# Optimization experiments

Hardware: AMD Instinct MI355X
Metric: run time of the kernel (lower is better)

The kernel has to match this reference:

```python
import jax, jax.numpy as jnp
import numpy as np

N_NODES = 50000
N_EDGES = 800000
N_GRAPHS = 256
F_IN = 75  # num_features_xd


def _lin_params(key, fan_in, fan_out):
    kw, kb = jax.random.split(key)
    s = 1.0 / np.sqrt(fan_in)
    W = jax.random.uniform(kw, (fan_in, fan_out), jnp.float32, -s, s)
    b = jax.random.uniform(kb, (fan_out,), jnp.float32, -s, s)
    return W, b


def setup_inputs() -> dict:
    key = jax.random.key(0)
    ks = jax.random.split(key, 8)
    x = jax.random.normal(ks[0], (N_NODES, F_IN), jnp.float32)
    edge_index = jax.random.randint(ks[1], (2, N_EDGES), 0, N_NODES, jnp.int32)
    batch = jnp.sort(jax.random.randint(ks[2], (N_NODES,), 0, N_GRAPHS, jnp.int32))
    W1, b1 = _lin_params(ks[3], F_IN, F_IN)            # conv1: 75 -> 75
    W2, b2 = _lin_params(ks[4], F_IN, 2 * F_IN)        # conv2: 75 -> 150
    W3, b3 = _lin_params(ks[5], 2 * F_IN, 4 * F_IN)    # conv3: 150 -> 300
    Wg1, bg1 = _lin_params(ks[6], 4 * F_IN, 1024)      # fc_g1: 300 -> 1024
    Wg2, bg2 = _lin_params(ks[7], 1024, 128)           # fc_g2: 1024 -> 128
    return dict(x=x, edge_index=edge_index, batch=batch,
                W1=W1, b1=b1, W2=W2, b2=b2, W3=W3, b3=b3,
                Wg1=Wg1, bg1=bg1, Wg2=Wg2, bg2=bg2)


def gcn_conv(x, W, b, src, dst, n):
    """PyG GCNConv: out = D^{-1/2}(A+I)D^{-1/2} X W + b (symmetric norm, self loops)."""
    h = x @ W                                   # [n, out]
    loop = jnp.arange(n, dtype=src.dtype)
    s = jnp.concatenate([src, loop])            # [E+n]
    d = jnp.concatenate([dst, loop])
    deg = jax.ops.segment_sum(jnp.ones(s.shape[0], x.dtype), d, num_segments=n)
    dinv = jnp.where(deg > 0, jax.lax.rsqrt(jnp.maximum(deg, 1e-12)), 0.0)
    norm = dinv[s] * dinv[d]                    # [E+n]
    out = jax.ops.segment_sum(norm[:, None] * h[s], d, num_segments=n)
    return out + b


def reference(x, edge_index, batch, W1, b1, W2, b2, W3, b3, Wg1, bg1, Wg2, bg2):
    src, dst = edge_index[0], edge_index[1]
    n = x.shape[0]
    h = jax.nn.relu(gcn_conv(x, W1, b1, src, dst, n))
    h = jax.nn.relu(gcn_conv(h, W2, b2, src, dst, n))
    h = jax.nn.relu(gcn_conv(h, W3, b3, src, dst, n))
    g = jax.ops.segment_max(h, batch, num_segments=N_GRAPHS)  # global max pool
    g = jax.nn.relu(g @ Wg1 + bg1)
    # dropout is identity in eval mode
    return g @ Wg2 + bg2
```

## Files before the change

### kernel.cpp

```cpp
#include <hip/hip_runtime.h>
#include <math.h>

#define SCAN_B 1024
#define LDST 40

typedef __attribute__((ext_vector_type(8))) short short8v;
typedef __attribute__((ext_vector_type(8))) unsigned short ushort8v;
typedef __attribute__((ext_vector_type(4))) float f32x4;

static inline int ceil_div_i(long long a, int b) { return (int)((a + b - 1) / b); }

__device__ __forceinline__ unsigned short f2bf(float x) {
    unsigned int u = __float_as_uint(x);
    u += 0x7fffu + ((u >> 16) & 1u);
    return (unsigned short)(u >> 16);
}
__device__ __forceinline__ float bf2f(unsigned short h) {
    return __uint_as_float(((unsigned int)h) << 16);
}


__global__ __launch_bounds__(256) void k_count(const int* __restrict__ dst, int E,
                                               int* __restrict__ cnt) {
    int i = blockIdx.x * blockDim.x + threadIdx.x;
    if (i < E) atomicAdd(&cnt[dst[i]], 1);
}

__global__ __launch_bounds__(256) void k_dinv(const int* __restrict__ cnt,
                                              float* __restrict__ dinv, int N) {
    int i = blockIdx.x * blockDim.x + threadIdx.x;
    if (i < N) dinv[i] = (float)(1.0 / sqrt((double)(cnt[i] + 1)));
}

__global__ __launch_bounds__(256) void k_scan1(const int* __restrict__ cnt,
                                               int* __restrict__ rowptr,
                                               int* __restrict__ bsum, int N) {
    __shared__ int s[256];
    int tid = threadIdx.x;
    int base = blockIdx.x * SCAN_B + tid * 4;
    int a0 = (base + 0 < N) ? cnt[base + 0] : 0;
    int a1 = (base + 1 < N) ? cnt[base + 1] : 0;
    int a2 = (base + 2 < N) ? cnt[base + 2] : 0;
    int a3 = (base + 3 < N) ? cnt[base + 3] : 0;
    int tsum = a0 + a1 + a2 + a3;
    s[tid] = tsum;
    __syncthreads();
    for (int off = 1; off < 256; off <<= 1) {
        int val = 0;
        if (tid >= off) val = s[tid - off];
        __syncthreads();
        if (tid >= off) s[tid] += val;
        __syncthreads();
    }
    int texcl = s[tid] - tsum;
    if (tid == 255) bsum[blockIdx.x] = s[255];
    if (base + 0 < N) rowptr[base + 0] = texcl;
    if (base + 1 < N) rowptr[base + 1] = texcl + a0;
    if (base + 2 < N) rowptr[base + 2] = texcl + a0 + a1;
    if (base + 3 < N) rowptr[base + 3] = texcl + a0 + a1 + a2;
}

__global__ __launch_bounds__(256) void k_scan2(int* __restrict__ bsum, int NB) {
    __shared__ int s[256];
    int tid = threadIdx.x;
    int v = (tid < NB) ? bsum[tid] : 0;
    s[tid] = v;
    __syncthreads();
    for (int off = 1; off < 256; off <<= 1) {
        int val = 0;
        if (tid >= off) val = s[tid - off];
        __syncthreads();
        if (tid >= off) s[tid] += val;
        __syncthreads();
    }
    if (tid < NB) bsum[tid] = s[tid] - v;
}

__global__ __launch_bounds__(256) void k_scan3(int* __restrict__ rowptr,
                                               const int* __restrict__ bsum, int N, int E) {
    int i = blockIdx.x * blockDim.x + threadIdx.x;
    if (i < N) rowptr[i] += bsum[i >> 10];
    if (i == 0) rowptr[N] = E;
}

__global__ __launch_bounds__(256) void k_fill(const int* __restrict__ src,
                                              const int* __restrict__ dst, int E,
                                              const int* __restrict__ rowptr,
                                              int* __restrict__ fill,
                                              const float* __restrict__ dinv,
                                              int* __restrict__ col,
                                              float* __restrict__ ew) {
    int e = blockIdx.x * blockDim.x + threadIdx.x;
    if (e >= E) return;
    int s = src[e], d = dst[e];
    int pos = atomicAdd(&fill[d], 1);
    int idx = rowptr[d] + pos;
    col[idx] = s;
    ew[idx] = dinv[s] * dinv[d];
}


__global__ __launch_bounds__(256) void k_xpad(const float* __restrict__ x,
                                              float* __restrict__ xp, int N, int F, int XS) {
    int i = blockIdx.x * blockDim.x + threadIdx.x;
    int v = i / XS, c = i - v * XS;
    if (v >= N) return;
    xp[i] = (c < F) ? x[(size_t)v * F + c] : 0.f;
}


template <int BF16IN, int CHUNKS, int SLOTS, int UNR>
__global__ __launch_bounds__(256) void k_gather_s(const void* __restrict__ Xv,
                                                  const int* __restrict__ rowptr,
                                                  const int* __restrict__ col,
                                                  const float* __restrict__ ew,
                                                  const float* __restrict__ dinv,
                                                  float* __restrict__ T, int N,
                                                  int XS, int KPf) {
    const int v = blockIdx.x * 4 + (threadIdx.x >> 6);
    const int lane = threadIdx.x & 63;
    if (v >= N) return;
    constexpr int VW = BF16IN ? 8 : 4;
    const int slot = lane / CHUNKS;
    const int chunk = lane - slot * CHUNKS;
    const bool act = lane < CHUNKS * SLOTS;
    const int f0 = chunk * VW;
    const float* Xf = (const float*)Xv;
    const unsigned short* Xb = (const unsigned short*)Xv;
    const float dv = dinv[v];
    const float s = dv * dv;

    float acc[VW];
#pragma unroll
    for (int u = 0; u < VW; u++) acc[u] = 0.f;
    if (slot == 0) {
        if (BF16IN) {
            ushort8v h = *(const ushort8v*)(Xb + (size_t)v * XS + f0);
#pragma unroll
            for (int u = 0; u < VW; u++) acc[u] = s * bf2f(h[u]);
        } else {
            f32x4 t4 = *(const f32x4*)(Xf + (size_t)v * XS + f0);
#pragma unroll
            for (int u = 0; u < VW; u++) acc[u] = s * t4[u];
        }
    }

    const int beg = rowptr[v], end = rowptr[v + 1];
    for (int jb = beg; jb < end; jb += 64) {
        const int nj = min(64, end - jb);
        int ec = 0;
        float emeta = 0.f;
        if (lane < nj) {
            ec = col[jb + lane];
            emeta = ew[jb + lane];
        }
        for (int e = 0; e < nj; e += SLOTS * UNR) {
            int cs[UNR];
            float ws[UNR];
            bool vs[UNR];
#pragma unroll
            for (int u = 0; u < UNR; u++) {
                int srcl = e + u * SLOTS + slot;
                vs[u] = act && (srcl < nj);
                int sl = srcl & 63;
                cs[u] = __shfl(ec, sl);
                ws[u] = __shfl(emeta, sl);
                if (!vs[u]) ws[u] = 0.f;
            }
            if (BF16IN) {
                ushort8v xv[UNR];
#pragma unroll
                for (int u = 0; u < UNR; u++) {
#pragma unroll
                    for (int k2 = 0; k2 < 8; k2++) xv[u][k2] = 0;
                    if (vs[u]) xv[u] = *(const ushort8v*)(Xb + (size_t)cs[u] * XS + f0);
                }
#pragma unroll
                for (int u = 0; u < UNR; u++)
#pragma unroll
                    for (int k2 = 0; k2 < VW; k2++)
                        acc[k2] = fmaf(ws[u], bf2f(xv[u][k2]), acc[k2]);
            } else {
                f32x4 xv[UNR];
#pragma unroll
                for (int u = 0; u < UNR; u++) {
                    xv[u] = (f32x4){0.f, 0.f, 0.f, 0.f};
                    if (vs[u]) xv[u] = *(const f32x4*)(Xf + (size_t)cs[u] * XS + f0);
                }
#pragma unroll
                for (int u = 0; u < UNR; u++)
#pragma unroll
                    for (int k2 = 0; k2 < VW; k2++)
                        acc[k2] = fmaf(ws[u], xv[u][k2], acc[k2]);
            }
        }
    }

#pragma unroll
    for (int k2 = 0; k2 < VW; k2++) {
        float t2 = acc[k2];
#pragma unroll
        for (int s2 = 1; s2 < SLOTS; s2++) t2 += __shfl(acc[k2], chunk + s2 * CHUNKS);
        acc[k2] = t2;
    }

    if (slot == 0 && f0 < KPf) {
        float* tv = T + (size_t)v * KPf + f0;
        f32x4 o0 = {acc[0], acc[1], acc[2], acc[3]};
        *(f32x4*)tv = o0;
        if (VW == 8) {
            f32x4 o1 = {acc[4], acc[5], acc[6], acc[7]};
            *(f32x4*)(tv + 4) = o1;
        }
    }
}


__global__ __launch_bounds__(256) void k_wsplit(const float* __restrict__ W,
                                                unsigned short* __restrict__ Wth,
                                                unsigned short* __restrict__ Wtl,
                                                int K, int Fout, int KP) {
    int i = blockIdx.x * blockDim.x + threadIdx.x;
    if (i >= Fout * KP) return;
    int c = i / KP, k = i - c * KP;
    float w = (k < K) ? W[(size_t)k * Fout + c] : 0.f;
    unsigned short h = f2bf(w);
    Wth[i] = h;
    Wtl[i] = f2bf(w - bf2f(h));
}


template <int MODE>
__global__ __launch_bounds__(256) void k_gemm_mfma(
    const float* __restrict__ A, int KPf,
    const unsigned short* __restrict__ Bth, const unsigned short* __restrict__ Btl,
    const float* __restrict__ bias, unsigned short* __restrict__ Cb, int CSbf,
    const int* __restrict__ batch, float* __restrict__ G,
    int N, int KP, int Fout) {
    __shared__ unsigned short sAh[128 * LDST];
    __shared__ unsigned short sAl[128 * LDST];
    __shared__ unsigned short sBh[128 * LDST];
    __shared__ unsigned short sBl[128 * LDST];
    __shared__ int sBatch[128];

    const int t = threadIdx.x;
    const int r0 = blockIdx.x * 128;
    const int c0 = blockIdx.y * 128;
    const int lane = t & 63;
    const int wv = t >> 6;
    const int wrow = (wv >> 1) * 64;
    const int wcol = (wv & 1) * 64;
    const int l15 = lane & 15;
    const int lk = (lane >> 4) * 8;
    const int nt = KP >> 5;

    const int srow = t >> 1;
    const int sseg = (t & 1) << 4;

    if (MODE == 1 && t < 128) sBatch[t] = (r0 + t < N) ? batch[r0 + t] : -1;

    const bool arow_ok = (r0 + srow) < N;
    const bool bcol_ok = (c0 + srow) < Fout;
    const float* aRow = A + (size_t)(r0 + srow) * KPf;
    const unsigned short* bhRow = Bth + (size_t)(c0 + srow) * KP;
    const unsigned short* blRow = Btl + (size_t)(c0 + srow) * KP;

    float av[16];
    ushort8v rbh0, rbh1, rbl0, rbl1;

    auto gload = [&](int kk) {
#pragma unroll
        for (int u = 0; u < 4; u++) {
            int gk = kk + sseg + u * 4;
            f32x4 f = {0.f, 0.f, 0.f, 0.f};
            if (arow_ok && gk < KPf) f = *(const f32x4*)&aRow[gk];
#pragma unroll
            for (int e = 0; e < 4; e++) av[u * 4 + e] = f[e];
        }
        if (bcol_ok) {
            const ushort8v* p = (const ushort8v*)&bhRow[kk + sseg];
            rbh0 = p[0];
            rbh1 = p[1];
            p = (const ushort8v*)&blRow[kk + sseg];
            rbl0 = p[0];
            rbl1 = p[1];
        } else {
#pragma unroll
            for (int e = 0; e < 8; e++) { rbh0[e] = 0; rbh1[e] = 0; rbl0[e] = 0; rbl1[e] = 0; }
        }
    };

    auto wlds = [&]() {
        int off = srow * LDST + sseg;
        ushort8v h0, h1, l0, l1;
#pragma unroll
        for (int e = 0; e < 8; e++) {
            unsigned short hh = f2bf(av[e]);
            h0[e] = hh;
            l0[e] = f2bf(av[e] - bf2f(hh));
        }
#pragma unroll
        for (int e = 0; e < 8; e++) {
            unsigned short hh = f2bf(av[8 + e]);
            h1[e] = hh;
            l1[e] = f2bf(av[8 + e] - bf2f(hh));
        }
        *(ushort8v*)&sAh[off] = h0;
        *(ushort8v*)&sAh[off + 8] = h1;
        *(ushort8v*)&sAl[off] = l0;
        *(ushort8v*)&sAl[off + 8] = l1;
        *(ushort8v*)&sBh[off] = rbh0;
        *(ushort8v*)&sBh[off + 8] = rbh1;
        *(ushort8v*)&sBl[off] = rbl0;
        *(ushort8v*)&sBl[off + 8] = rbl1;
    };

    f32x4 acc[4][4];
#pragma unroll
    for (int i = 0; i < 4; i++)
#pragma unroll
        for (int j = 0; j < 4; j++) acc[i][j] = (f32x4){0.f, 0.f, 0.f, 0.f};

    gload(0);
    for (int tc = 0; tc < nt; ++tc) {
        wlds();
        __syncthreads();
        if (tc + 1 < nt) gload((tc + 1) * 32);
        short8v ah[4], al[4];
#pragma unroll
        for (int i = 0; i < 4; i++) {
            int ro = (wrow + i * 16 + l15) * LDST + lk;
            ah[i] = *(const short8v*)&sAh[ro];
            al[i] = *(const short8v*)&sAl[ro];
        }
#pragma unroll
        for (int j = 0; j < 4; j++) {
            int co = (wcol + j * 16 + l15) * LDST + lk;
            short8v bh = *(const short8v*)&sBh[co];
            short8v bl = *(const short8v*)&sBl[co];
#pragma unroll
            for (int i = 0; i < 4; i++) {
                acc[i][j] = __builtin_amdgcn_mfma_f32_16x16x32_bf16(al[i], bh, acc[i][j], 0, 0, 0);
                acc[i][j] = __builtin_amdgcn_mfma_f32_16x16x32_bf16(ah[i], bl, acc[i][j], 0, 0, 0);
                acc[i][j] = __builtin_amdgcn_mfma_f32_16x16x32_bf16(ah[i], bh, acc[i][j], 0, 0, 0);
            }
        }
        __syncthreads();
    }

    if (MODE == 0) {
#pragma unroll
        for (int j = 0; j < 4; j++) {
            int gc = c0 + wcol + j * 16 + l15;
            if (gc >= CSbf) continue;
            float bv = (gc < Fout) ? bias[gc] : 0.f;
#pragma unroll
            for (int i = 0; i < 4; i++) {
                int rb = r0 + wrow + i * 16 + (lane >> 4) * 4;
#pragma unroll
                for (int q = 0; q < 4; q++) {
                    int gr = rb + q;
                    if (gr >= N) continue;
                    float vv = (gc < Fout) ? fmaxf(acc[i][j][q] + bv, 0.f) : 0.f;
                    Cb[(size_t)gr * CSbf + gc] = f2bf(vv);
                }
            }
        }
    } else {
#pragma unroll
        for (int j = 0; j < 4; j++) {
            int gc = c0 + wcol + j * 16 + l15;
            if (gc >= Fout) continue;
            float bv = bias[gc];
            int gcur = -1;
            float vmax = 0.f;
#pragma unroll
            for (int i = 0; i < 4; i++) {
                int lr = wrow + i * 16 + (lane >> 4) * 4;
#pragma unroll
                for (int q = 0; q < 4; q++) {
                    int g = sBatch[lr + q];
                    float vv = fmaxf(acc[i][j][q] + bv, 0.f);
                    if (g < 0) continue;
                    if (g != gcur) {
                        if (gcur >= 0)
                            atomicMax((int*)&G[(size_t)gcur * Fout + gc], __float_as_int(vmax));
                        gcur = g;
                        vmax = vv;
                    } else {
                        vmax = fmaxf(vmax, vv);
                    }
                }
            }
            if (gcur >= 0) atomicMax((int*)&G[(size_t)gcur * Fout + gc], __float_as_int(vmax));
        }
    }
}


__global__ __launch_bounds__(256) void k_fc1(const float* __restrict__ A,
                                             const float* __restrict__ W,
                                             const float* __restrict__ bias,
                                             float* __restrict__ C,
                                             int M, int K, int Nout) {
    __shared__ float sA[2 * 304];
    const int t = threadIdx.x;
    const int m0 = blockIdx.x * 2;
    const int oc = blockIdx.y * 256 + t;

    for (int i = t; i < 2 * K; i += 256) {
        int r = i / K, k = i - r * K;
        sA[r * 304 + k] = (m0 + r < M) ? A[(size_t)(m0 + r) * K + k] : 0.f;
    }
    __syncthreads();

    float acc0 = 0.f, acc1 = 0.f;
    int k = 0;
    for (; k + 8 <= K; k += 8) {
        float w[8];
#pragma unroll
        for (int u = 0; u < 8; u++) w[u] = W[(size_t)(k + u) * Nout + oc];
#pragma unroll
        for (int u = 0; u < 8; u++) {
            acc0 = fmaf(sA[k + u], w[u], acc0);
            acc1 = fmaf(sA[304 + k + u], w[u], acc1);
        }
    }
    for (; k < K; k++) {
        float w = W[(size_t)k * Nout + oc];
        acc0 = fmaf(sA[k], w, acc0);
        acc1 = fmaf(sA[304 + k], w, acc1);
    }
    float bv = bias[oc];
    if (m0 < M) C[(size_t)m0 * Nout + oc] = fmaxf(acc0 + bv, 0.f);
    if (m0 + 1 < M) C[(size_t)(m0 + 1) * Nout + oc] = fmaxf(acc1 + bv, 0.f);
}


__global__ __launch_bounds__(256) void k_fc2p(const float* __restrict__ A,
                                              const float* __restrict__ W,
                                              float* __restrict__ P,
                                              int M, int K, int Nout) {
    __shared__ float sA[2 * 256];
    const int t = threadIdx.x;
    const int m0 = blockIdx.x * 2;
    const int sk = blockIdx.y;
    const int k0 = sk * 256;
    const int row = t >> 7;
    const int oc = t & 127;

    for (int i = t; i < 2 * 256; i += 256) {
        int r = i >> 8, k = i & 255;
        sA[i] = (m0 + r < M) ? A[(size_t)(m0 + r) * K + k0 + k] : 0.f;
    }
    __syncthreads();

    const float* a = sA + row * 256;
    float acc = 0.f;
    for (int k = 0; k < 256; k += 8) {
        float w[8];
#pragma unroll
        for (int u = 0; u < 8; u++) w[u] = W[(size_t)(k0 + k + u) * Nout + oc];
#pragma unroll
        for (int u = 0; u < 8; u++) acc = fmaf(a[k + u], w[u], acc);
    }
    int m = m0 + row;
    if (m < M) P[((size_t)sk * M + m) * Nout + oc] = acc;
}

__global__ __launch_bounds__(256) void k_fc2r(const float* __restrict__ P,
                                              const float* __restrict__ bias,
                                              float* __restrict__ C,
                                              int M, int Nout, int SK) {
    int i = blockIdx.x * blockDim.x + threadIdx.x;
    if (i >= M * Nout) return;
    int oc = i % Nout;
    float acc = bias[oc];
    for (int s2 = 0; s2 < SK; s2++) acc += P[(size_t)s2 * M * Nout + i];
    C[i] = acc;
}


extern "C" void kernel_launch(void* const* d_in, const int* in_sizes, int n_in,
                              void* d_out, int out_size, void* d_ws, size_t ws_size,
                              hipStream_t stream) {
    const float* x     = (const float*)d_in[0];
    const int*   ei    = (const int*)d_in[1];
    const int*   batch = (const int*)d_in[2];
    const float* W1 = (const float*)d_in[3];
    const float* b1 = (const float*)d_in[4];
    const float* W2 = (const float*)d_in[5];
    const float* b2 = (const float*)d_in[6];
    const float* W3 = (const float*)d_in[7];
    const float* b3 = (const float*)d_in[8];
    const float* Wg1 = (const float*)d_in[9];
    const float* bg1 = (const float*)d_in[10];
    const float* Wg2 = (const float*)d_in[11];
    const float* bg2 = (const float*)d_in[12];

    const int N  = in_sizes[2];
    const int E  = in_sizes[1] / 2;
    const int F1 = in_sizes[4];
    const int F2 = in_sizes[6];
    const int F3 = in_sizes[8];
    const int H1 = in_sizes[10];
    const int OC = in_sizes[12];
    const int NG = out_size / OC;
    const int FIN = in_sizes[3] / F1;

    const int KP1 = 96,  KPf1 = 80;
    const int KP3 = 160, KPf3 = 152;
    const int XSP = 76;
    const int HS1 = 80;
    const int HS2 = 152;

    const int* src = ei;
    const int* dst = ei + E;

    char* base = (char*)d_ws;
    size_t off = 0;
    auto alloc = [&](size_t bytes) -> void* {
        void* p = base + off;
        off = (off + bytes + 255) & ~(size_t)255;
        return p;
    };
    int*   cnt    = (int*)alloc((size_t)N * 4);
    int*   fill   = (int*)alloc((size_t)N * 4);
    int*   rowptr = (int*)alloc((size_t)(N + 1) * 4);
    float* dinv   = (float*)alloc((size_t)N * 4);
    int*   bsum   = (int*)alloc(256 * 4);
    int*   col    = (int*)alloc((size_t)E * 4);
    float* ew     = (float*)alloc((size_t)E * 4);
    unsigned short* W1th = (unsigned short*)alloc((size_t)F1 * KP1 * 2);
    unsigned short* W1tl = (unsigned short*)alloc((size_t)F1 * KP1 * 2);
    unsigned short* W2th = (unsigned short*)alloc((size_t)F2 * KP1 * 2);
    unsigned short* W2tl = (unsigned short*)alloc((size_t)F2 * KP1 * 2);
    unsigned short* W3th = (unsigned short*)alloc((size_t)F3 * KP3 * 2);
    unsigned short* W3tl = (unsigned short*)alloc((size_t)F3 * KP3 * 2);
    float* Gb  = (float*)alloc((size_t)NG * F3 * 4);
    float* g1  = (float*)alloc((size_t)NG * H1 * 4);
    float* P2  = (float*)alloc((size_t)4 * NG * OC * 4);
    float* Tg  = (float*)alloc((size_t)N * KPf3 * 4);
    float* xp  = (float*)alloc((size_t)N * XSP * 4);
    unsigned short* H1b = (unsigned short*)alloc((size_t)N * HS1 * 2);
    unsigned short* H2b = (unsigned short*)alloc((size_t)N * HS2 * 2);

    hipMemsetAsync(cnt, 0, (size_t)N * 4, stream);
    hipMemsetAsync(fill, 0, (size_t)N * 4, stream);
    hipMemsetAsync(Gb, 0, (size_t)NG * F3 * 4, stream);

    k_count<<<ceil_div_i(E, 256), 256, 0, stream>>>(dst, E, cnt);
    k_dinv<<<ceil_div_i(N, 256), 256, 0, stream>>>(cnt, dinv, N);
    int NB = ceil_div_i(N, SCAN_B);
    k_scan1<<<NB, 256, 0, stream>>>(cnt, rowptr, bsum, N);
    k_scan2<<<1, 256, 0, stream>>>(bsum, NB);
    k_scan3<<<ceil_div_i(N, 256), 256, 0, stream>>>(rowptr, bsum, N, E);
    k_fill<<<ceil_div_i(E, 256), 256, 0, stream>>>(src, dst, E, rowptr, fill, dinv, col, ew);

    k_wsplit<<<ceil_div_i((long long)F1 * KP1, 256), 256, 0, stream>>>(W1, W1th, W1tl, FIN, F1, KP1);
    k_wsplit<<<ceil_div_i((long long)F2 * KP1, 256), 256, 0, stream>>>(W2, W2th, W2tl, F1, F2, KP1);
    k_wsplit<<<ceil_div_i((long long)F3 * KP3, 256), 256, 0, stream>>>(W3, W3th, W3tl, F2, F3, KP3);
    k_xpad<<<ceil_div_i((long long)N * XSP, 256), 256, 0, stream>>>(x, xp, N, FIN, XSP);

    dim3 blk(256);
    int gw = ceil_div_i(N, 4);
    int gx = ceil_div_i(N, 128);

    k_gather_s<0, 19, 3, 4><<<gw, blk, 0, stream>>>(xp, rowptr, col, ew, dinv, Tg,
                                                    N, XSP, KPf1);
    {
        dim3 g(gx, ceil_div_i(F1, 128));
        k_gemm_mfma<0><<<g, blk, 0, stream>>>(Tg, KPf1, W1th, W1tl, b1, H1b, HS1,
                                              nullptr, nullptr, N, KP1, F1);
    }
    k_gather_s<1, 10, 6, 2><<<gw, blk, 0, stream>>>(H1b, rowptr, col, ew, dinv, Tg,
                                                    N, HS1, KPf1);
    {
        dim3 g(gx, ceil_div_i(F2, 128));
        k_gemm_mfma<0><<<g, blk, 0, stream>>>(Tg, KPf1, W2th, W2tl, b2, H2b, HS2,
                                              nullptr, nullptr, N, KP1, F2);
    }
    k_gather_s<1, 19, 3, 4><<<gw, blk, 0, stream>>>(H2b, rowptr, col, ew, dinv, Tg,
                                                    N, HS2, KPf3);
    {
        dim3 g(gx, ceil_div_i(F3, 128));
        k_gemm_mfma<1><<<g, blk, 0, stream>>>(Tg, KPf3, W3th, W3tl, b3, nullptr, 0,
                                              batch, Gb, N, KP3, F3);
    }

    {
        dim3 g(ceil_div_i(NG, 2), H1 / 256);
        k_fc1<<<g, 256, 0, stream>>>(Gb, Wg1, bg1, g1, NG, F3, H1);
    }
    {
        dim3 g(ceil_div_i(NG, 2), 4);
        k_fc2p<<<g, 256, 0, stream>>>(g1, Wg2, P2, NG, H1, OC);
        k_fc2r<<<ceil_div_i((long long)NG * OC, 256), 256, 0, stream>>>(
            P2, bg2, (float*)d_out, NG, OC, 4);
    }
}
```

Baseline: 356.6 us.

## Fold symmetric GCN normalization into node features, drop per-edge weights

Factors the D^-1/2 A D^-1/2 normalization into per-node scaling: inputs are pre-scaled by dinv, the gather just sums neighbor rows, and the GEMM epilogue multiplies by dinv before bias and again after ReLU for the next layer. This removes the per-edge weight array, its writes in k_fill, its reads and shuffles in every gather, and turns FMAs into adds. The first-layer input is also converted to bf16 (stride 80), which halves gather traffic for layer 1 but adds rounding error on the raw input.

```diff
diff --git a/kernel.cpp b/kernel.cpp
--- a/kernel.cpp
+++ b/kernel.cpp
@@ -87,112 +87,77 @@
                                               const int* __restrict__ dst, int E,
                                               const int* __restrict__ rowptr,
                                               int* __restrict__ fill,
-                                              const float* __restrict__ dinv,
-                                              int* __restrict__ col,
-                                              float* __restrict__ ew) {
+                                              int* __restrict__ col) {
     int e = blockIdx.x * blockDim.x + threadIdx.x;
     if (e >= E) return;
     int s = src[e], d = dst[e];
     int pos = atomicAdd(&fill[d], 1);
-    int idx = rowptr[d] + pos;
-    col[idx] = s;
-    ew[idx] = dinv[s] * dinv[d];
-}
-
-
-__global__ __launch_bounds__(256) void k_xpad(const float* __restrict__ x,
-                                              float* __restrict__ xp, int N, int F, int XS) {
+    col[rowptr[d] + pos] = s;
+}
+
+
+__global__ __launch_bounds__(256) void k_xscale(const float* __restrict__ x,
+                                                const float* __restrict__ dinv,
+                                                unsigned short* __restrict__ xb,
+                                                int N, int F, int XS) {
     int i = blockIdx.x * blockDim.x + threadIdx.x;
     int v = i / XS, c = i - v * XS;
     if (v >= N) return;
-    xp[i] = (c < F) ? x[(size_t)v * F + c] : 0.f;
-}
-
-
-template <int BF16IN, int CHUNKS, int SLOTS, int UNR>
-__global__ __launch_bounds__(256) void k_gather_s(const void* __restrict__ Xv,
+    float val = (c < F) ? dinv[v] * x[(size_t)v * F + c] : 0.f;
+    xb[i] = f2bf(val);
+}
+
+
+template <int CHUNKS, int SLOTS, int UNR>
+__global__ __launch_bounds__(256) void k_gather_s(const unsigned short* __restrict__ Xb,
                                                   const int* __restrict__ rowptr,
                                                   const int* __restrict__ col,
-                                                  const float* __restrict__ ew,
-                                                  const float* __restrict__ dinv,
                                                   float* __restrict__ T, int N,
                                                   int XS, int KPf) {
     const int v = blockIdx.x * 4 + (threadIdx.x >> 6);
     const int lane = threadIdx.x & 63;
     if (v >= N) return;
-    constexpr int VW = BF16IN ? 8 : 4;
+    constexpr int VW = 8;
     const int slot = lane / CHUNKS;
     const int chunk = lane - slot * CHUNKS;
     const bool act = lane < CHUNKS * SLOTS;
     const int f0 = chunk * VW;
-    const float* Xf = (const float*)Xv;
-    const unsigned short* Xb = (const unsigned short*)Xv;
-    const float dv = dinv[v];
-    const float s = dv * dv;
 
     float acc[VW];
 #pragma unroll
     for (int u = 0; u < VW; u++) acc[u] = 0.f;
     if (slot == 0) {
-        if (BF16IN) {
-            ushort8v h = *(const ushort8v*)(Xb + (size_t)v * XS + f0);
-#pragma unroll
-            for (int u = 0; u < VW; u++) acc[u] = s * bf2f(h[u]);
-        } else {
-            f32x4 t4 = *(const f32x4*)(Xf + (size_t)v * XS + f0);
-#pragma unroll
-            for (int u = 0; u < VW; u++) acc[u] = s * t4[u];
-        }
+        ushort8v h = *(const ushort8v*)(Xb + (size_t)v * XS + f0);
+#pragma unroll
+        for (int u = 0; u < VW; u++) acc[u] = bf2f(h[u]);
     }
 
     const int beg = rowptr[v], end = rowptr[v + 1];
     for (int jb = beg; jb < end; jb += 64) {
         const int nj = min(64, end - jb);
         int ec = 0;
-        float emeta = 0.f;
-        if (lane < nj) {
-            ec = col[jb + lane];
-            emeta = ew[jb + lane];
-        }
+        if (lane < nj) ec = col[jb + lane];
         for (int e = 0; e < nj; e += SLOTS * UNR) {
             int cs[UNR];
-            float ws[UNR];
             bool vs[UNR];
 #pragma unroll
             for (int u = 0; u < UNR; u++) {
                 int srcl = e + u * SLOTS + slot;
                 vs[u] = act && (srcl < nj);
-                int sl = srcl & 63;
-                cs[u] = __shfl(ec, sl);
-                ws[u] = __shfl(emeta, sl);
-                if (!vs[u]) ws[u] = 0.f;
+                cs[u] = __shfl(ec, srcl & 63);
             }
-            if (BF16IN) {
-                ushort8v xv[UNR];
-#pragma unroll
-                for (int u = 0; u < UNR; u++) {
-#pragma unroll
-                    for (int k2 = 0; k2 < 8; k2++) xv[u][k2] = 0;
-                    if (vs[u]) xv[u] = *(const ushort8v*)(Xb + (size_t)cs[u] * XS + f0);
-                }
-#pragma unroll
-                for (int u = 0; u < UNR; u++)
-#pragma unroll
-                    for (int k2 = 0; k2 < VW; k2++)
-                        acc[k2] = fmaf(ws[u], bf2f(xv[u][k2]), acc[k2]);
-            } else {
-                f32x4 xv[UNR];
-#pragma unroll
-                for (int u = 0; u < UNR; u++) {
-                    xv[u] = (f32x4){0.f, 0.f, 0.f, 0.f};
-                    if (vs[u]) xv[u] = *(const f32x4*)(Xf + (size_t)cs[u] * XS + f0);
-                }
-#pragma unroll
-                for (int u = 0; u < UNR; u++)
-#pragma unroll
-                    for (int k2 = 0; k2 < VW; k2++)
-                        acc[k2] = fmaf(ws[u], xv[u][k2], acc[k2]);
+            ushort8v xv[UNR];
+#pragma unroll
+            for (int u = 0; u < UNR; u++) {
+#pragma unroll
+                for (int k2 = 0; k2 < 8; k2++) xv[u][k2] = 0;
+                if (vs[u]) xv[u] = *(const ushort8v*)(Xb + (size_t)cs[u] * XS + f0);
             }
+#pragma unroll
+            for (int u = 0; u < UNR; u++)
+#pragma unroll
+                for (int k2 = 0; k2 < VW; k2++)
+                    acc[k2] += bf2f(xv[u][k2]);
         }
     }
 
@@ -207,11 +172,9 @@
     if (slot == 0 && f0 < KPf) {
         float* tv = T + (size_t)v * KPf + f0;
         f32x4 o0 = {acc[0], acc[1], acc[2], acc[3]};
+        f32x4 o1 = {acc[4], acc[5], acc[6], acc[7]};
         *(f32x4*)tv = o0;
-        if (VW == 8) {
-            f32x4 o1 = {acc[4], acc[5], acc[6], acc[7]};
-            *(f32x4*)(tv + 4) = o1;
-        }
+        *(f32x4*)(tv + 4) = o1;
     }
 }
 
@@ -234,7 +197,8 @@
 __global__ __launch_bounds__(256) void k_gemm_mfma(
     const float* __restrict__ A, int KPf,
     const unsigned short* __restrict__ Bth, const unsigned short* __restrict__ Btl,
-    const float* __restrict__ bias, unsigned short* __restrict__ Cb, int CSbf,
+    const float* __restrict__ bias, const float* __restrict__ dinvp,
+    unsigned short* __restrict__ Cb, int CSbf,
     const int* __restrict__ batch, float* __restrict__ G,
     int N, int KP, int Fout) {
     __shared__ unsigned short sAh[128 * LDST];
@@ -348,6 +312,15 @@
         __syncthreads();
     }
 
+    float drw[16];
+#pragma unroll
+    for (int i = 0; i < 4; i++)
+#pragma unroll
+        for (int q = 0; q < 4; q++) {
+            int gr = r0 + wrow + i * 16 + (lane >> 4) * 4 + q;
+            drw[i * 4 + q] = (gr < N) ? dinvp[gr] : 0.f;
+        }
+
     if (MODE == 0) {
 #pragma unroll
         for (int j = 0; j < 4; j++) {
@@ -361,7 +334,8 @@
                 for (int q = 0; q < 4; q++) {
                     int gr = rb + q;
                     if (gr >= N) continue;
-                    float vv = (gc < Fout) ? fmaxf(acc[i][j][q] + bv, 0.f) : 0.f;
+                    float dr = drw[i * 4 + q];
+                    float vv = (gc < Fout) ? fmaxf(fmaf(acc[i][j][q], dr, bv), 0.f) * dr : 0.f;
                     Cb[(size_t)gr * CSbf + gc] = f2bf(vv);
                 }
             }
@@ -380,7 +354,7 @@
 #pragma unroll
                 for (int q = 0; q < 4; q++) {
                     int g = sBatch[lr + q];
-                    float vv = fmaxf(acc[i][j][q] + bv, 0.f);
+                    float vv = fmaxf(fmaf(acc[i][j][q], drw[i * 4 + q], bv), 0.f);
                     if (g < 0) continue;
                     if (g != gcur) {
                         if (gcur >= 0)
@@ -510,7 +484,7 @@
 
     const int KP1 = 96,  KPf1 = 80;
     const int KP3 = 160, KPf3 = 152;
-    const int XSP = 76;
+    const int XS0 = 80;
     const int HS1 = 80;
     const int HS2 = 152;
 
@@ -530,7 +504,6 @@
     float* dinv   = (float*)alloc((size_t)N * 4);
     int*   bsum   = (int*)alloc(256 * 4);
     int*   col    = (int*)alloc((size_t)E * 4);
-    float* ew     = (float*)alloc((size_t)E * 4);
     unsigned short* W1th = (unsigned short*)alloc((size_t)F1 * KP1 * 2);
     unsigned short* W1tl = (unsigned short*)alloc((size_t)F1 * KP1 * 2);
     unsigned short* W2th = (unsigned short*)alloc((size_t)F2 * KP1 * 2);
@@ -541,7 +514,7 @@
     float* g1  = (float*)alloc((size_t)NG * H1 * 4);
     float* P2  = (float*)alloc((size_t)4 * NG * OC * 4);
     float* Tg  = (float*)alloc((size_t)N * KPf3 * 4);
-    float* xp  = (float*)alloc((size_t)N * XSP * 4);
+    unsigned short* Xb  = (unsigned short*)alloc((size_t)N * XS0 * 2);
     unsigned short* H1b = (unsigned short*)alloc((size_t)N * HS1 * 2);
     unsigned short* H2b = (unsigned short*)alloc((size_t)N * HS2 * 2);
 
@@ -555,36 +528,33 @@
     k_scan1<<<NB, 256, 0, stream>>>(cnt, rowptr, bsum, N);
     k_scan2<<<1, 256, 0, stream>>>(bsum, NB);
     k_scan3<<<ceil_div_i(N, 256), 256, 0, stream>>>(rowptr, bsum, N, E);
-    k_fill<<<ceil_div_i(E, 256), 256, 0, stream>>>(src, dst, E, rowptr, fill, dinv, col, ew);
+    k_fill<<<ceil_div_i(E, 256), 256, 0, stream>>>(src, dst, E, rowptr, fill, col);
 
     k_wsplit<<<ceil_div_i((long long)F1 * KP1, 256), 256, 0, stream>>>(W1, W1th, W1tl, FIN, F1, KP1);
     k_wsplit<<<ceil_div_i((long long)F2 * KP1, 256), 256, 0, stream>>>(W2, W2th, W2tl, F1, F2, KP1);
     k_wsplit<<<ceil_div_i((long long)F3 * KP3, 256), 256, 0, stream>>>(W3, W3th, W3tl, F2, F3, KP3);
-    k_xpad<<<ceil_div_i((long long)N * XSP, 256), 256, 0, stream>>>(x, xp, N, FIN, XSP);
+    k_xscale<<<ceil_div_i((long long)N * XS0, 256), 256, 0, stream>>>(x, dinv, Xb, N, FIN, XS0);
 
     dim3 blk(256);
     int gw = ceil_div_i(N, 4);
     int gx = ceil_div_i(N, 128);
 
-    k_gather_s<0, 19, 3, 4><<<gw, blk, 0, stream>>>(xp, rowptr, col, ew, dinv, Tg,
-                                                    N, XSP, KPf1);
+    k_gather_s<10, 6, 2><<<gw, blk, 0, stream>>>(Xb, rowptr, col, Tg, N, XS0, KPf1);
     {
         dim3 g(gx, ceil_div_i(F1, 128));
-        k_gemm_mfma<0><<<g, blk, 0, stream>>>(Tg, KPf1, W1th, W1tl, b1, H1b, HS1,
+        k_gemm_mfma<0><<<g, blk, 0, stream>>>(Tg, KPf1, W1th, W1tl, b1, dinv, H1b, HS1,
                                               nullptr, nullptr, N, KP1, F1);
     }
-    k_gather_s<1, 10, 6, 2><<<gw, blk, 0, stream>>>(H1b, rowptr, col, ew, dinv, Tg,
-                                                    N, HS1, KPf1);
+    k_gather_s<10, 6, 2><<<gw, blk, 0, stream>>>(H1b, rowptr, col, Tg, N, HS1, KPf1);
     {
         dim3 g(gx, ceil_div_i(F2, 128));
-        k_gemm_mfma<0><<<g, blk, 0, stream>>>(Tg, KPf1, W2th, W2tl, b2, H2b, HS2,
+        k_gemm_mfma<0><<<g, blk, 0, stream>>>(Tg, KPf1, W2th, W2tl, b2, dinv, H2b, HS2,
                                               nullptr, nullptr, N, KP1, F2);
     }
-    k_gather_s<1, 19, 3, 4><<<gw, blk, 0, stream>>>(H2b, rowptr, col, ew, dinv, Tg,
-                                                    N, HS2, KPf3);
+    k_gather_s<19, 3, 4><<<gw, blk, 0, stream>>>(H2b, rowptr, col, Tg, N, HS2, KPf3);
     {
         dim3 g(gx, ceil_div_i(F3, 128));
-        k_gemm_mfma<1><<<g, blk, 0, stream>>>(Tg, KPf3, W3th, W3tl, b3, nullptr, 0,
+        k_gemm_mfma<1><<<g, blk, 0, stream>>>(Tg, KPf3, W3th, W3tl, b3, dinv, nullptr, 0,
                                               batch, Gb, N, KP3, F3);
     }
 
```

Result: faster. 336.3 us (-5.7%).
